# Optimization experiments

Measured on AMD Instinct MI355X. Metric: run time of the kernel, lower is better.

## Reference

```python
import jax, jax.numpy as jnp
import numpy as np

B, C, L, H, W = 8, 64, 32, 64, 64

def setup_inputs() -> dict:
    key = jax.random.key(0)
    k1, k2, k3, k4, k5 = jax.random.split(key, 5)
    inpt = jax.random.normal(k1, (B, C, L, H, W), dtype=jnp.float32)
    # 1x1x1 conv kernels collapse to per-channel vectors
    theta_w = jax.random.normal(k2, (C,), dtype=jnp.float32) * 0.1  # Conv3d(c,1,1) weight
    g_w = jax.random.normal(k3, (C,), dtype=jnp.float32) * 0.1      # Conv3d(c,1,1) weight
    h_w = jax.random.normal(k4, (C,), dtype=jnp.float32) * 0.1      # Conv3d(1,c,1) weight
    h_b = jax.random.normal(k5, (C,), dtype=jnp.float32) * 0.1      # Conv3d(1,c,1) bias
    return {"inpt": inpt, "theta_w": theta_w, "g_w": g_w, "h_w": h_w, "h_b": h_b}

def reference(inpt, theta_w, g_w, h_w, h_b):
    b, c, l, h, w = inpt.shape
    # theta/g: 1x1x1 convs c->1 == channel contraction
    t = jnp.einsum('bclhw,c->blhw', inpt, theta_w).reshape(b, -1)  # (b, N)
    g = jnp.einsum('bclhw,c->blhw', inpt, g_w).reshape(b, -1)      # (b, N)
    # outer product t[b,1,N]*g[b,N,1] followed by AvgPool1d(N) over last axis
    # == g scaled by mean(t); skip the O(N^2) intermediate entirely
    mt = jnp.mean(t, axis=1, keepdims=True)                        # (b, 1)
    x = (g * mt).reshape(b, 1, l, h, w)
    # h: 1x1x1 conv 1->c with bias
    y = x * h_w[None, :, None, None, None] + h_b[None, :, None, None, None]
    return inpt + y
```

## Files before the change

### kernel.cpp

```cpp
#include <hip/hip_runtime.h>

#define BB 8
#define CC 64
#define NSP 131072
#define PPB 512

__global__ __launch_bounds__(256) void k_pipe(
    const float* __restrict__ inpt, const float* __restrict__ theta_w,
    const float* __restrict__ g_w, const float* __restrict__ h_w,
    const float* __restrict__ h_b, float* __restrict__ out,
    float* __restrict__ partials, int b_k1, int b_k3)
{
    if (blockIdx.x < PPB) {
        if (b_k1 >= BB) return;
        int blk = blockIdx.x;
        int bc  = (b_k1 << 6) + (blk >> 3);
        int q   = blk & 7;
        const float4* base = reinterpret_cast<const float4*>(inpt)
                             + (((size_t)bc) << 15) + ((size_t)q << 12);
        float4 s4 = make_float4(0.f, 0.f, 0.f, 0.f);
        #pragma unroll
        for (int i = 0; i < 16; ++i) {
            float4 x = base[i * 256 + threadIdx.x];
            s4.x += x.x; s4.y += x.y; s4.z += x.z; s4.w += x.w;
        }
        float s = (s4.x + s4.y) + (s4.z + s4.w);
        #pragma unroll
        for (int off = 32; off > 0; off >>= 1) s += __shfl_down(s, off);
        __shared__ float red[4];
        int wid = threadIdx.x >> 6;
        if ((threadIdx.x & 63) == 0) red[wid] = s;
        __syncthreads();
        if (threadIdx.x == 0)
            partials[(b_k1 << 9) + blk] = (red[0] + red[1]) + (red[2] + red[3]);
    } else {
        if (b_k3 < 0) return;
        int blk  = (int)blockIdx.x - PPB;
        int lane = threadIdx.x & 63;

        const float* p = partials + (b_k3 << 9);
        float v = 0.f;
        #pragma unroll
        for (int i = 0; i < 8; ++i) {
            int idx = i * 64 + lane;
            v = fmaf(p[idx], theta_w[idx >> 3], v);
        }
        #pragma unroll
        for (int off = 32; off > 0; off >>= 1) v += __shfl_down(v, off);
        float mt = __shfl(v, 0) * (1.0f / (float)NSP);

        size_t n = ((size_t)blk << 8) + threadIdx.x;
        const float* base  = inpt + (((size_t)b_k3) << 23) + n;
        float vals[CC];
        float gacc = 0.f;
        #pragma unroll
        for (int c = 0; c < CC; ++c) {
            vals[c] = base[((size_t)c) << 17];
            gacc = fmaf(vals[c], g_w[c], gacc);
        }
        float sc = gacc * mt;
        float* obase = out + (((size_t)b_k3) << 23) + n;
        #pragma unroll
        for (int c = 0; c < CC; ++c) {
            float o = fmaf(sc, h_w[c], vals[c] + h_b[c]);
            __builtin_nontemporal_store(o, obase + (((size_t)c) << 17));
        }
    }
}

extern "C" void kernel_launch(void* const* d_in, const int* in_sizes, int n_in,
                              void* d_out, int out_size, void* d_ws, size_t ws_size,
                              hipStream_t stream)
{
    const float* inpt    = (const float*)d_in[0];
    const float* theta_w = (const float*)d_in[1];
    const float* g_w     = (const float*)d_in[2];
    const float* h_w     = (const float*)d_in[3];
    const float* h_b     = (const float*)d_in[4];
    float* out = (float*)d_out;

    float* partials = (float*)d_ws;

    for (int s = 0; s <= BB; ++s) {
        hipLaunchKernelGGL(k_pipe, dim3(2 * PPB), dim3(256), 0, stream,
                           inpt, theta_w, g_w, h_w, h_b, out, partials,
                           s, s - 1);
    }
}
```

Baseline: 150.9 us.

## Replace per-batch pipelined launches with two whole-tensor kernels and float2 accesses

Drops the nine-launch software pipeline, in which each launch reduced one batch while applying the output for the previous batch. It now runs one reduction kernel over all batches, then one apply kernel over all batches in which each thread handles two spatial positions with float2 loads and stores. This removes launch overhead and the partially idle grids at the pipeline's first and last launches. It gives up the L2 reuse the pipeline had, where a batch slice just read for the sum could still be cached when the apply pass read it again. With a 256 MiB input, the apply pass will likely refetch from HBM.

```diff
diff --git a/kernel.cpp b/kernel.cpp
--- a/kernel.cpp
+++ b/kernel.cpp
@@ -3,68 +3,74 @@
 #define BB 8
 #define CC 64
 #define NSP 131072
-#define PPB 512
+#define QPB 8
+#define NPART (BB * CC * QPB)
 
-__global__ __launch_bounds__(256) void k_pipe(
+typedef float f2v __attribute__((ext_vector_type(2)));
+
+__global__ __launch_bounds__(256) void k1_sum(
+    const float* __restrict__ inpt, float* __restrict__ partials)
+{
+    int blk = blockIdx.x;
+    int bc = blk >> 3, q = blk & 7;
+    const float4* base = reinterpret_cast<const float4*>(inpt)
+                         + (((size_t)bc) << 15) + (q << 12);
+    float4 s4 = make_float4(0.f, 0.f, 0.f, 0.f);
+    #pragma unroll
+    for (int i = 0; i < 16; ++i) {
+        float4 x = base[i * 256 + threadIdx.x];
+        s4.x += x.x; s4.y += x.y; s4.z += x.z; s4.w += x.w;
+    }
+    float s = (s4.x + s4.y) + (s4.z + s4.w);
+    #pragma unroll
+    for (int off = 32; off > 0; off >>= 1) s += __shfl_down(s, off);
+    __shared__ float red[4];
+    int wid = threadIdx.x >> 6;
+    if ((threadIdx.x & 63) == 0) red[wid] = s;
+    __syncthreads();
+    if (threadIdx.x == 0) partials[blk] = (red[0] + red[1]) + (red[2] + red[3]);
+}
+
+__global__ __launch_bounds__(256) void k3_fused2(
     const float* __restrict__ inpt, const float* __restrict__ theta_w,
     const float* __restrict__ g_w, const float* __restrict__ h_w,
-    const float* __restrict__ h_b, float* __restrict__ out,
-    float* __restrict__ partials, int b_k1, int b_k3)
+    const float* __restrict__ h_b, const float* __restrict__ partials,
+    float* __restrict__ out)
 {
-    if (blockIdx.x < PPB) {
-        if (b_k1 >= BB) return;
-        int blk = blockIdx.x;
-        int bc  = (b_k1 << 6) + (blk >> 3);
-        int q   = blk & 7;
-        const float4* base = reinterpret_cast<const float4*>(inpt)
-                             + (((size_t)bc) << 15) + ((size_t)q << 12);
-        float4 s4 = make_float4(0.f, 0.f, 0.f, 0.f);
-        #pragma unroll
-        for (int i = 0; i < 16; ++i) {
-            float4 x = base[i * 256 + threadIdx.x];
-            s4.x += x.x; s4.y += x.y; s4.z += x.z; s4.w += x.w;
-        }
-        float s = (s4.x + s4.y) + (s4.z + s4.w);
-        #pragma unroll
-        for (int off = 32; off > 0; off >>= 1) s += __shfl_down(s, off);
-        __shared__ float red[4];
-        int wid = threadIdx.x >> 6;
-        if ((threadIdx.x & 63) == 0) red[wid] = s;
-        __syncthreads();
-        if (threadIdx.x == 0)
-            partials[(b_k1 << 9) + blk] = (red[0] + red[1]) + (red[2] + red[3]);
-    } else {
-        if (b_k3 < 0) return;
-        int blk  = (int)blockIdx.x - PPB;
-        int lane = threadIdx.x & 63;
+    size_t idx2 = (size_t)blockIdx.x * 256 + threadIdx.x;
+    int b = (int)(idx2 >> 16);
+    int lane = threadIdx.x & 63;
 
-        const float* p = partials + (b_k3 << 9);
-        float v = 0.f;
-        #pragma unroll
-        for (int i = 0; i < 8; ++i) {
-            int idx = i * 64 + lane;
-            v = fmaf(p[idx], theta_w[idx >> 3], v);
-        }
-        #pragma unroll
-        for (int off = 32; off > 0; off >>= 1) v += __shfl_down(v, off);
-        float mt = __shfl(v, 0) * (1.0f / (float)NSP);
+    const float* p = partials + (b << 9);
+    float v = 0.f;
+    #pragma unroll
+    for (int i = 0; i < 8; ++i) {
+        int pi = i * 64 + lane;
+        v = fmaf(p[pi], theta_w[pi >> 3], v);
+    }
+    #pragma unroll
+    for (int off = 32; off > 0; off >>= 1) v += __shfl_down(v, off);
+    float mt = __shfl(v, 0) * (1.0f / (float)NSP);
 
-        size_t n = ((size_t)blk << 8) + threadIdx.x;
-        const float* base  = inpt + (((size_t)b_k3) << 23) + n;
-        float vals[CC];
-        float gacc = 0.f;
-        #pragma unroll
-        for (int c = 0; c < CC; ++c) {
-            vals[c] = base[((size_t)c) << 17];
-            gacc = fmaf(vals[c], g_w[c], gacc);
-        }
-        float sc = gacc * mt;
-        float* obase = out + (((size_t)b_k3) << 23) + n;
-        #pragma unroll
-        for (int c = 0; c < CC; ++c) {
-            float o = fmaf(sc, h_w[c], vals[c] + h_b[c]);
-            __builtin_nontemporal_store(o, obase + (((size_t)c) << 17));
-        }
+    size_t n2 = idx2 & 65535;
+    const f2v* base = reinterpret_cast<const f2v*>(inpt)
+                      + ((((size_t)b) << 6) << 16) + n2;
+    f2v vals[CC];
+    float gx = 0.f, gy = 0.f;
+    #pragma unroll
+    for (int c = 0; c < CC; ++c) {
+        vals[c] = base[((size_t)c) << 16];
+        gx = fmaf(vals[c].x, g_w[c], gx);
+        gy = fmaf(vals[c].y, g_w[c], gy);
+    }
+    float sx = gx * mt, sy = gy * mt;
+    f2v* obase = reinterpret_cast<f2v*>(out) + ((((size_t)b) << 6) << 16) + n2;
+    #pragma unroll
+    for (int c = 0; c < CC; ++c) {
+        f2v o;
+        o.x = fmaf(sx, h_w[c], vals[c].x + h_b[c]);
+        o.y = fmaf(sy, h_w[c], vals[c].y + h_b[c]);
+        __builtin_nontemporal_store(o, obase + (((size_t)c) << 16));
     }
 }
 
@@ -81,9 +87,8 @@
 
     float* partials = (float*)d_ws;
 
-    for (int s = 0; s <= BB; ++s) {
-        hipLaunchKernelGGL(k_pipe, dim3(2 * PPB), dim3(256), 0, stream,
-                           inpt, theta_w, g_w, h_w, h_b, out, partials,
-                           s, s - 1);
-    }
+    hipLaunchKernelGGL(k1_sum, dim3(NPART), dim3(256), 0, stream,
+                       inpt, partials);
+    hipLaunchKernelGGL(k3_fused2, dim3((BB * NSP / 2) / 256), dim3(256), 0, stream,
+                       inpt, theta_w, g_w, h_w, h_b, partials, out);
 }
```

New measurement: 122.2 us. 1.23x faster.
